# Kernel tuning notes

Measured on AMD Instinct MI355X. Metric: run time of the kernel, lower is better.

The kernel has to match this reference:

```python
import jax, jax.numpy as jnp
import numpy as np

DIM = 3072
NUM_HEADS = 24
HEAD_DIM = 128
INNER = NUM_HEADS * HEAD_DIM
EPS = 1e-5


def _layernorm(x, eps=EPS):
    # affine-free LayerNorm over the last (head_dim) axis
    mu = jnp.mean(x, axis=-1, keepdims=True)
    var = jnp.mean(jnp.square(x - mu), axis=-1, keepdims=True)
    return (x - mu) * jax.lax.rsqrt(var + eps)


def _rope_interleaved(x, cos, sin):
    # x: (B, S_img, H, D); cos/sin: (S_img, D//2). Non-neox (interleaved) style.
    x1 = x[..., 0::2]
    x2 = x[..., 1::2]
    c = cos[None, :, None, :]
    s = sin[None, :, None, :]
    o1 = x1 * c - x2 * s
    o2 = x2 * c + x1 * s
    return jnp.stack([o1, o2], axis=-1).reshape(x.shape)


def setup_inputs() -> dict:
    key = jax.random.key(0)
    ks = jax.random.split(key, 8)
    B, S_txt, S_img = 1, 256, 2048
    hidden_states = jax.random.normal(ks[0], (B, S_img, DIM), dtype=jnp.float32)
    encoder_hidden_states = jax.random.normal(ks[1], (B, S_txt, DIM), dtype=jnp.float32)
    cos = jax.random.uniform(ks[2], (S_img, HEAD_DIM // 2), dtype=jnp.float32)
    sin = jax.random.uniform(ks[3], (S_img, HEAD_DIM // 2), dtype=jnp.float32)
    Wqkv = jax.random.normal(ks[4], (DIM, 3 * INNER), dtype=jnp.float32) * (DIM ** -0.5)
    bqkv = jnp.zeros((3 * INNER,), dtype=jnp.float32)
    Wout = jax.random.normal(ks[5], (INNER, DIM), dtype=jnp.float32) * (INNER ** -0.5)
    bout = jnp.zeros((DIM,), dtype=jnp.float32)
    return {
        "hidden_states": hidden_states,
        "encoder_hidden_states": encoder_hidden_states,
        "cos": cos,
        "sin": sin,
        "Wqkv": Wqkv,
        "bqkv": bqkv,
        "Wout": Wout,
        "bout": bout,
        "text_seq_length": 256,
    }


def reference(hidden_states, encoder_hidden_states, cos, sin, Wqkv, bqkv, Wout, bout, text_seq_length):
    T = text_seq_length
    x = jnp.concatenate([encoder_hidden_states, hidden_states], axis=1)  # (B, S, dim)
    B, S, _ = x.shape
    qkv = x @ Wqkv + bqkv  # (B, S, 3*inner)
    q, k, v = jnp.split(qkv, 3, axis=-1)
    q = q.reshape(B, S, NUM_HEADS, HEAD_DIM)
    k = k.reshape(B, S, NUM_HEADS, HEAD_DIM)
    v = v.reshape(B, S, NUM_HEADS, HEAD_DIM)
    q = _layernorm(q)
    k = _layernorm(k)
    # partial RoPE: only on image-token slice
    q = jnp.concatenate([q[:, :T], _rope_interleaved(q[:, T:], cos, sin)], axis=1)
    k = jnp.concatenate([k[:, :T], _rope_interleaved(k[:, T:], cos, sin)], axis=1)
    scale = 1.0 / (HEAD_DIM ** 0.5)
    scores = jnp.einsum("bqhd,bkhd->bhqk", q, k) * scale
    probs = jax.nn.softmax(scores, axis=-1)
    out = jnp.einsum("bhqk,bkhd->bqhd", probs, v)
    out = out.reshape(B, S, INNER)
    out = out @ Wout + bout
    encoder_out = out[:, :T, :]
    hidden_out = out[:, T:, :]
    return (hidden_out, encoder_out)
```

## Files before the change

kernel.cpp:

```cpp
#include <hip/hip_runtime.h>

#define DIMC 3072
#define NH 24
#define HD 128
#define QKV_N 9216
#define S_TXT 256
#define S_IMG 2048
#define S_TOT 2304

typedef _Float16 f16x8 __attribute__((ext_vector_type(8)));
typedef _Float16 f16x4 __attribute__((ext_vector_type(4)));
typedef _Float16 f16x2 __attribute__((ext_vector_type(2)));
typedef float f32x4 __attribute__((ext_vector_type(4)));

#define MFMA(A, B, C) __builtin_amdgcn_mfma_f32_16x16x32_f16(A, B, C, 0, 0, 0)

#define QSCALE (0.08838834764831845f * 1.4426950408889634f)

__device__ __forceinline__ void gl2lds16(const _Float16* g, _Float16* l) {
    __builtin_amdgcn_global_load_lds(
        (const __attribute__((address_space(1))) unsigned int*)g,
        (__attribute__((address_space(3))) unsigned int*)l,
        16, 0, 0);
}

__global__ __launch_bounds__(256) void split_x(
    const float* __restrict__ enc, const float* __restrict__ hid,
    _Float16* __restrict__ xh)
{
    const int s = blockIdx.x;
    const float* src = (s < S_TXT) ? enc + (size_t)s * DIMC
                                   : hid + (size_t)(s - S_TXT) * DIMC;
    const int t = threadIdx.x;
#pragma unroll
    for (int it = 0; it < 3; ++it) {
        const int i = (it * 256 + t) * 4;
        float4 v = *(const float4*)(src + i);
        f16x4 hv;
        hv.x = (_Float16)v.x; hv.y = (_Float16)v.y;
        hv.z = (_Float16)v.z; hv.w = (_Float16)v.w;
        *(f16x4*)(xh + (size_t)s * DIMC + i) = hv;
    }
}

__global__ __launch_bounds__(256) void transpose_w_hi(
    const float* __restrict__ W, const int ldw, _Float16* __restrict__ Th)
{
    __shared__ float T[64][68];
    const int n0 = blockIdx.x * 64, k0 = blockIdx.y * 64;
    const int t = threadIdx.x;
    {
        const int r = t >> 2, c4 = (t & 3) * 16;
#pragma unroll
        for (int j = 0; j < 4; ++j) {
            float4 v = *(const float4*)(W + (size_t)(k0 + r) * ldw + n0 + c4 + j * 4);
            *(float4*)&T[r][c4 + j * 4] = v;
        }
    }
    __syncthreads();
    const int nr = t >> 2, kp = (t & 3) * 16;
    f16x8 hv0, hv1;
#pragma unroll
    for (int j = 0; j < 8; ++j) hv0[j] = (_Float16)T[kp + j][nr];
#pragma unroll
    for (int j = 0; j < 8; ++j) hv1[j] = (_Float16)T[kp + 8 + j][nr];
    _Float16* dh = Th + (size_t)(n0 + nr) * DIMC + k0 + kp;
    *(f16x8*)(dh) = hv0; *(f16x8*)(dh + 8) = hv1;
}

template <int REMAP>
__global__ __launch_bounds__(256) void gemm_f16_lds(
    const _Float16* __restrict__ Ah, const _Float16* __restrict__ Bh,
    const float* __restrict__ bias, float* __restrict__ C,
    const int nblk_m, const int ldc)
{
    __shared__ __attribute__((aligned(16))) _Float16 Ash[128 * 32];
    __shared__ __attribute__((aligned(16))) _Float16 Bsh[128 * 32];

    const int cpx = (int)gridDim.x >> 3;
    const int wgid = (blockIdx.x & 7) * cpx + (blockIdx.x >> 3);
    const int bm = (wgid % nblk_m) * 128;
    const int bn = (wgid / nblk_m) * 128;

    const int tid = threadIdx.x;
    const int l = tid & 63, w = tid >> 6;
    const int wr = w >> 1, wc = w & 1;
    const int lr = l & 15, g = l >> 4;

    const int srow0 = w * 32 + (l >> 2);
    const int srow1 = srow0 + 16;
    const int skp0 = (((l & 3) ^ ((srow0 >> 1) & 3)) * 8);
    const int skp1 = (((l & 3) ^ ((srow1 >> 1) & 3)) * 8);
    const _Float16* gA0 = Ah + (size_t)(bm + srow0) * DIMC + skp0;
    const _Float16* gA1 = Ah + (size_t)(bm + srow1) * DIMC + skp1;
    const _Float16* gB0 = Bh + (size_t)(bn + srow0) * DIMC + skp0;
    const _Float16* gB1 = Bh + (size_t)(bn + srow1) * DIMC + skp1;
    _Float16* lA0 = &Ash[(w * 32) * 32];
    _Float16* lA1 = &Ash[(w * 32 + 16) * 32];
    _Float16* lB0 = &Bsh[(w * 32) * 32];
    _Float16* lB1 = &Bsh[(w * 32 + 16) * 32];

    int aoff[4], boff[4];
#pragma unroll
    for (int i = 0; i < 4; ++i) {
        const int ra = wr * 64 + i * 16 + lr;
        const int rb = wc * 64 + i * 16 + lr;
        aoff[i] = ra * 32 + ((g ^ ((ra >> 1) & 3)) * 8);
        boff[i] = rb * 32 + ((g ^ ((rb >> 1) & 3)) * 8);
    }

    f32x4 acc[4][4] = {};

    for (int k0 = 0; k0 < DIMC; k0 += 32) {
        gl2lds16(gA0 + k0, lA0);
        gl2lds16(gA1 + k0, lA1);
        gl2lds16(gB0 + k0, lB0);
        gl2lds16(gB1 + k0, lB1);
        __syncthreads();

        f16x8 bhf[4];
#pragma unroll
        for (int ni = 0; ni < 4; ++ni)
            bhf[ni] = *(const f16x8*)&Bsh[boff[ni]];
#pragma unroll
        for (int mi = 0; mi < 4; ++mi) {
            f16x8 ahf = *(const f16x8*)&Ash[aoff[mi]];
#pragma unroll
            for (int ni = 0; ni < 4; ++ni)
                acc[mi][ni] = MFMA(ahf, bhf[ni], acc[mi][ni]);
        }
        __syncthreads();
    }

#pragma unroll
    for (int mi = 0; mi < 4; ++mi)
#pragma unroll
        for (int ni = 0; ni < 4; ++ni) {
            const int cl = bn + wc * 64 + ni * 16 + lr;
            const float bv = bias[cl];
#pragma unroll
            for (int e = 0; e < 4; ++e) {
                const int r = bm + wr * 64 + mi * 16 + g * 4 + e;
                if (REMAP) {
                    const int gr = (r < S_TXT) ? (S_IMG + r) : (r - S_TXT);
                    C[(size_t)gr * DIMC + cl] = acc[mi][ni][e] + bv;
                } else {
                    C[(size_t)r * ldc + cl] = acc[mi][ni][e] + bv;
                }
            }
        }
}

__global__ __launch_bounds__(256) void ln_rope_split(
    const float* __restrict__ qkv,
    const float* __restrict__ cost, const float* __restrict__ sint,
    _Float16* __restrict__ Qh, _Float16* __restrict__ Kh)
{
    const int wave = threadIdx.x >> 6;
    const int lane = threadIdx.x & 63;
    const int task = blockIdx.x * 4 + wave;
    const int s = task / 48;
    const int rem = task % 48;
    const int qk = rem / 24;
    const int h = rem % 24;

    const float* p = qkv + (size_t)s * QKV_N + qk * DIMC + h * HD;
    float2 x = *(const float2*)(p + lane * 2);

    float sum = x.x + x.y;
    float sq = x.x * x.x + x.y * x.y;
#pragma unroll
    for (int off = 1; off < 64; off <<= 1) {
        sum += __shfl_xor(sum, off, 64);
        sq  += __shfl_xor(sq, off, 64);
    }
    const float mu = sum * (1.0f / 128.0f);
    const float var = sq * (1.0f / 128.0f) - mu * mu;
    const float rstd = rsqrtf(var + 1e-5f);
    float y0 = (x.x - mu) * rstd;
    float y1 = (x.y - mu) * rstd;

    if (s >= S_TXT) {
        const int ip = s - S_TXT;
        const float c = cost[ip * 64 + lane];
        const float sn = sint[ip * 64 + lane];
        const float o0 = y0 * c - y1 * sn;
        const float o1 = y1 * c + y0 * sn;
        y0 = o0; y1 = o1;
    }
    if (qk == 0) { y0 *= QSCALE; y1 *= QSCALE; }

    const size_t off = ((size_t)h * S_TOT + s) * HD + lane * 2;
    f16x2 hv; hv.x = (_Float16)y0; hv.y = (_Float16)y1;
    *(f16x2*)((qk ? Kh : Qh) + off) = hv;
}

__global__ __launch_bounds__(256) void v_split_transpose(
    const float* __restrict__ qkv, _Float16* __restrict__ Vth)
{
    __shared__ float T[64][132];
    const int h = blockIdx.y;
    const int s0 = blockIdx.x * 64;
    const int t = threadIdx.x;
    {
        const int sl = t >> 2, dp = (t & 3) * 32;
#pragma unroll
        for (int j = 0; j < 8; ++j) {
            float4 v = *(const float4*)(qkv + (size_t)(s0 + sl) * QKV_N + 2 * DIMC + h * HD + dp + j * 4);
            *(float4*)&T[sl][dp + j * 4] = v;
        }
    }
    __syncthreads();
    const int d = t >> 1, sh = (t & 1) * 32;
    f16x8 hv[4];
#pragma unroll
    for (int ss = 0; ss < 32; ++ss)
        hv[ss >> 3][ss & 7] = (_Float16)T[sh + ss][d];
    _Float16* bh = Vth + ((size_t)h * HD + d) * S_TOT + s0 + sh;
#pragma unroll
    for (int j = 0; j < 4; ++j)
        *(f16x8*)(bh + j * 8) = hv[j];
}

__global__ __launch_bounds__(256) void attn_mfma(
    const _Float16* __restrict__ Qg, const _Float16* __restrict__ Kg,
    const _Float16* __restrict__ Vg, _Float16* __restrict__ aoh)
{
    __shared__ __attribute__((aligned(16))) _Float16 Ksh[4][64][40];
    __shared__ __attribute__((aligned(16))) _Float16 Vsh[128][80];
    __shared__ __attribute__((aligned(16))) _Float16 Pah[4][16][80];

    const int h = blockIdx.y;
    const int q0 = blockIdx.x * 64;
    const int tid = threadIdx.x;
    const int w = tid >> 6, l = tid & 63;
    const int lr = l & 15, g = l >> 4, lk = g * 8;

    const int qrow = q0 + w * 16 + lr;
    const _Float16* qb = Qg + ((size_t)h * S_TOT + qrow) * HD + lk;
    f16x8 qh[4];
#pragma unroll
    for (int db = 0; db < 4; ++db)
        qh[db] = *(const f16x8*)(qb + db * 32);

    f32x4 o[8] = {};
    float mrow = -3.0e38f, lrow = 0.0f;

    const int kkv = tid >> 2, kdb = tid & 3;
    const int vd = tid >> 1, vkh = (tid & 1) * 32;
    const _Float16* gK = Kg + ((size_t)h * S_TOT + kkv) * HD + kdb * 32;
    const _Float16* gV = Vg + ((size_t)h * HD + vd) * S_TOT + vkh;

    uint4 rK0, rK1, rK2, rK3, rV0, rV1, rV2, rV3;
#define LOADKV(kv0) { \
    rK0 = *(const uint4*)(gK + (size_t)(kv0) * HD);      rK1 = *(const uint4*)(gK + (size_t)(kv0) * HD + 8); \
    rK2 = *(const uint4*)(gK + (size_t)(kv0) * HD + 16); rK3 = *(const uint4*)(gK + (size_t)(kv0) * HD + 24); \
    rV0 = *(const uint4*)(gV + (kv0));      rV1 = *(const uint4*)(gV + (kv0) + 8); \
    rV2 = *(const uint4*)(gV + (kv0) + 16); rV3 = *(const uint4*)(gV + (kv0) + 24); }

    LOADKV(0);

    for (int kb = 0; kb < S_TOT / 64; ++kb) {
        __syncthreads();
        *(uint4*)&Ksh[kdb][kkv][0]  = rK0; *(uint4*)&Ksh[kdb][kkv][8]  = rK1;
        *(uint4*)&Ksh[kdb][kkv][16] = rK2; *(uint4*)&Ksh[kdb][kkv][24] = rK3;
        *(uint4*)&Vsh[vd][vkh]      = rV0; *(uint4*)&Vsh[vd][vkh + 8]  = rV1;
        *(uint4*)&Vsh[vd][vkh + 16] = rV2; *(uint4*)&Vsh[vd][vkh + 24] = rV3;
        __syncthreads();
        if (kb + 1 < S_TOT / 64) LOADKV((kb + 1) * 64);

        f32x4 sT[4] = {};
        __builtin_amdgcn_s_setprio(1);
#pragma unroll
        for (int db = 0; db < 4; ++db)
#pragma unroll
            for (int mf = 0; mf < 4; ++mf) {
                f16x8 kf = *(const f16x8*)&Ksh[db][mf * 16 + lr][lk];
                sT[mf] = MFMA(kf, qh[db], sT[mf]);
            }
        __builtin_amdgcn_s_setprio(0);

        float pm = -3.0e38f;
#pragma unroll
        for (int mf = 0; mf < 4; ++mf)
#pragma unroll
            for (int e = 0; e < 4; ++e)
                pm = fmaxf(pm, sT[mf][e]);
        pm = fmaxf(pm, __shfl_xor(pm, 16, 64));
        pm = fmaxf(pm, __shfl_xor(pm, 32, 64));

        if (__any(pm > mrow + 11.0f)) {
            const float mnew = fmaxf(mrow, pm);
            const float alpha = exp2f(mrow - mnew);
            lrow *= alpha;
            mrow = mnew;
            const float a0 = __shfl(alpha, g * 4 + 0, 64);
            const float a1 = __shfl(alpha, g * 4 + 1, 64);
            const float a2 = __shfl(alpha, g * 4 + 2, 64);
            const float a3 = __shfl(alpha, g * 4 + 3, 64);
#pragma unroll
            for (int df = 0; df < 8; ++df) {
                o[df][0] *= a0; o[df][1] *= a1; o[df][2] *= a2; o[df][3] *= a3;
            }
        }

        float rs = 0.0f;
        float ex_[4][4];
#pragma unroll
        for (int mf = 0; mf < 4; ++mf)
#pragma unroll
            for (int e = 0; e < 4; ++e) {
                const float pv = exp2f(sT[mf][e] - mrow);
                ex_[mf][e] = pv;
                rs += pv;
            }
        rs += __shfl_xor(rs, 16, 64);
        rs += __shfl_xor(rs, 32, 64);
        lrow += rs;

#pragma unroll
        for (int mf = 0; mf < 4; ++mf) {
            const int kvb = mf * 16 + g * 4;
            f16x2 t0; t0.x = (_Float16)ex_[mf][0]; t0.y = (_Float16)ex_[mf][1];
            f16x2 t1; t1.x = (_Float16)ex_[mf][2]; t1.y = (_Float16)ex_[mf][3];
            *(f16x2*)&Pah[w][lr][kvb] = t0;
            *(f16x2*)&Pah[w][lr][kvb + 2] = t1;
        }

        f16x8 pa0 = *(const f16x8*)&Pah[w][lr][lk];
        f16x8 pa1 = *(const f16x8*)&Pah[w][lr][32 + lk];
        __builtin_amdgcn_s_setprio(1);
#pragma unroll
        for (int df = 0; df < 8; ++df) {
            f16x8 vf0 = *(const f16x8*)&Vsh[df * 16 + lr][lk];
            f16x8 vf1 = *(const f16x8*)&Vsh[df * 16 + lr][32 + lk];
            o[df] = MFMA(pa0, vf0, o[df]);
            o[df] = MFMA(pa1, vf1, o[df]);
        }
        __builtin_amdgcn_s_setprio(0);
    }
#undef LOADKV

    const float inv = 1.0f / lrow;
    const float b0 = __shfl(inv, g * 4 + 0, 64);
    const float b1 = __shfl(inv, g * 4 + 1, 64);
    const float b2 = __shfl(inv, g * 4 + 2, 64);
    const float b3 = __shfl(inv, g * 4 + 3, 64);
    const float bb[4] = {b0, b1, b2, b3};
#pragma unroll
    for (int df = 0; df < 8; ++df)
#pragma unroll
        for (int e = 0; e < 4; ++e) {
            const int r = q0 + w * 16 + g * 4 + e;
            aoh[(size_t)r * DIMC + h * HD + df * 16 + lr] = (_Float16)(o[df][e] * bb[e]);
        }
}

extern "C" void kernel_launch(void* const* d_in, const int* in_sizes, int n_in,
                              void* d_out, int out_size, void* d_ws, size_t ws_size,
                              hipStream_t stream)
{
    const float* hid  = (const float*)d_in[0];
    const float* enc  = (const float*)d_in[1];
    const float* cost = (const float*)d_in[2];
    const float* sint = (const float*)d_in[3];
    const float* Wqkv = (const float*)d_in[4];
    const float* bqkv = (const float*)d_in[5];
    const float* Wout = (const float*)d_in[6];
    const float* bout = (const float*)d_in[7];
    float* out = (float*)d_out;

    char* ws = (char*)d_ws;
    float*    qkv  = (float*)(ws + 0);
    _Float16* aoh  = (_Float16*)(ws + 0);
    _Float16* xh   = (_Float16*)(ws + 84934656);
    _Float16* Qh   = (_Float16*)(ws + 84934656);
    _Float16* Kh   = (_Float16*)(ws + 99090432);
    _Float16* Wth  = (_Float16*)(ws + 113246208);
    _Float16* Vth  = (_Float16*)(ws + 113246208);
    _Float16* W2h  = (_Float16*)(ws + 132120576);

    split_x<<<S_TOT, 256, 0, stream>>>(enc, hid, xh);
    transpose_w_hi<<<dim3(144, 48), 256, 0, stream>>>(Wqkv, QKV_N, Wth);
    gemm_f16_lds<0><<<18 * 72, 256, 0, stream>>>(xh, Wth, bqkv, qkv, 18, QKV_N);
    transpose_w_hi<<<dim3(48, 48), 256, 0, stream>>>(Wout, DIMC, W2h);
    ln_rope_split<<<(S_TOT * 48) / 4, 256, 0, stream>>>(qkv, cost, sint, Qh, Kh);
    v_split_transpose<<<dim3(36, 24), 256, 0, stream>>>(qkv, Vth);
    attn_mfma<<<dim3(36, 24), 256, 0, stream>>>(Qh, Kh, Vth, aoh);
    gemm_f16_lds<1><<<18 * 24, 256, 0, stream>>>(aoh, W2h, bout, out, 18, DIMC);
}
```

Baseline: 477.4 us.

## Swizzle attention LDS layouts with XOR and remap blocks across XCDs

Replaces the padded K, V and P shared-memory arrays with unpadded arrays that use an XOR swizzle on 16-byte chunks. This avoids bank conflicts while cutting LDS footprint, which may allow more resident blocks per CU. It also flattens the grid to 1D and remaps block IDs so consecutive blocks of the same head land on the same XCD, to improve L2 reuse of K/V. The swizzle index math adds a few integer ops per access.

```diff
diff --git a/kernel.cpp b/kernel.cpp
--- a/kernel.cpp
+++ b/kernel.cpp
@@ -226,18 +226,19 @@
     const _Float16* __restrict__ Qg, const _Float16* __restrict__ Kg,
     const _Float16* __restrict__ Vg, _Float16* __restrict__ aoh)
 {
-    __shared__ __attribute__((aligned(16))) _Float16 Ksh[4][64][40];
-    __shared__ __attribute__((aligned(16))) _Float16 Vsh[128][80];
-    __shared__ __attribute__((aligned(16))) _Float16 Pah[4][16][80];
-
-    const int h = blockIdx.y;
-    const int q0 = blockIdx.x * 64;
+    __shared__ __attribute__((aligned(16))) _Float16 Ksh[4 * 64 * 32];
+    __shared__ __attribute__((aligned(16))) _Float16 Vsh[128 * 64];
+    __shared__ __attribute__((aligned(16))) _Float16 Pah[4 * 16 * 64];
+
+    const int wgid = ((int)blockIdx.x & 7) * 108 + ((int)blockIdx.x >> 3);
+    const int h = wgid / 36;
+    const int q0 = (wgid % 36) * 64;
     const int tid = threadIdx.x;
     const int w = tid >> 6, l = tid & 63;
-    const int lr = l & 15, g = l >> 4, lk = g * 8;
+    const int lr = l & 15, g = l >> 4;
 
     const int qrow = q0 + w * 16 + lr;
-    const _Float16* qb = Qg + ((size_t)h * S_TOT + qrow) * HD + lk;
+    const _Float16* qb = Qg + ((size_t)h * S_TOT + qrow) * HD + g * 8;
     f16x8 qh[4];
 #pragma unroll
     for (int db = 0; db < 4; ++db)
@@ -246,10 +247,23 @@
     f32x4 o[8] = {};
     float mrow = -3.0e38f, lrow = 0.0f;
 
+    const int kxr = (lr >> 1) & 3;
+    const int px  = lr & 7;
+    int ksl[4];
+#pragma unroll
+    for (int db = 0; db < 4; ++db) ksl[db] = (g ^ kxr ^ db) * 8;
+    const int vs0 = (g ^ px) * 8;
+    const int vs1 = ((4 + g) ^ px) * 8;
+
     const int kkv = tid >> 2, kdb = tid & 3;
-    const int vd = tid >> 1, vkh = (tid & 1) * 32;
+    const int vd = tid >> 1;
+    const int kx = (kkv >> 1) & 3;
+    const int kbase = kdb * 2048 + kkv * 32;
+    const int vbase = vd * 64;
+    const int vx = vd & 7;
+    const int vg0 = (tid & 1) * 4;
     const _Float16* gK = Kg + ((size_t)h * S_TOT + kkv) * HD + kdb * 32;
-    const _Float16* gV = Vg + ((size_t)h * HD + vd) * S_TOT + vkh;
+    const _Float16* gV = Vg + ((size_t)h * HD + vd) * S_TOT + (tid & 1) * 32;
 
     uint4 rK0, rK1, rK2, rK3, rV0, rV1, rV2, rV3;
 #define LOADKV(kv0) { \
@@ -262,10 +276,14 @@
 
     for (int kb = 0; kb < S_TOT / 64; ++kb) {
         __syncthreads();
-        *(uint4*)&Ksh[kdb][kkv][0]  = rK0; *(uint4*)&Ksh[kdb][kkv][8]  = rK1;
-        *(uint4*)&Ksh[kdb][kkv][16] = rK2; *(uint4*)&Ksh[kdb][kkv][24] = rK3;
-        *(uint4*)&Vsh[vd][vkh]      = rV0; *(uint4*)&Vsh[vd][vkh + 8]  = rV1;
-        *(uint4*)&Vsh[vd][vkh + 16] = rV2; *(uint4*)&Vsh[vd][vkh + 24] = rV3;
+        *(uint4*)&Ksh[kbase + ((0 ^ kx ^ kdb) * 8)] = rK0;
+        *(uint4*)&Ksh[kbase + ((1 ^ kx ^ kdb) * 8)] = rK1;
+        *(uint4*)&Ksh[kbase + ((2 ^ kx ^ kdb) * 8)] = rK2;
+        *(uint4*)&Ksh[kbase + ((3 ^ kx ^ kdb) * 8)] = rK3;
+        *(uint4*)&Vsh[vbase + (((vg0 + 0) ^ vx) * 8)] = rV0;
+        *(uint4*)&Vsh[vbase + (((vg0 + 1) ^ vx) * 8)] = rV1;
+        *(uint4*)&Vsh[vbase + (((vg0 + 2) ^ vx) * 8)] = rV2;
+        *(uint4*)&Vsh[vbase + (((vg0 + 3) ^ vx) * 8)] = rV3;
         __syncthreads();
         if (kb + 1 < S_TOT / 64) LOADKV((kb + 1) * 64);
 
@@ -275,7 +293,7 @@
         for (int db = 0; db < 4; ++db)
 #pragma unroll
             for (int mf = 0; mf < 4; ++mf) {
-                f16x8 kf = *(const f16x8*)&Ksh[db][mf * 16 + lr][lk];
+                f16x8 kf = *(const f16x8*)&Ksh[db * 2048 + (mf * 16 + lr) * 32 + ksl[db]];
                 sT[mf] = MFMA(kf, qh[db], sT[mf]);
             }
         __builtin_amdgcn_s_setprio(0);
@@ -318,22 +336,25 @@
         rs += __shfl_xor(rs, 32, 64);
         lrow += rs;
 
-#pragma unroll
-        for (int mf = 0; mf < 4; ++mf) {
-            const int kvb = mf * 16 + g * 4;
-            f16x2 t0; t0.x = (_Float16)ex_[mf][0]; t0.y = (_Float16)ex_[mf][1];
-            f16x2 t1; t1.x = (_Float16)ex_[mf][2]; t1.y = (_Float16)ex_[mf][3];
-            *(f16x2*)&Pah[w][lr][kvb] = t0;
-            *(f16x2*)&Pah[w][lr][kvb + 2] = t1;
-        }
-
-        f16x8 pa0 = *(const f16x8*)&Pah[w][lr][lk];
-        f16x8 pa1 = *(const f16x8*)&Pah[w][lr][32 + lk];
+        {
+            const int pbase = w * 1024 + lr * 64;
+#pragma unroll
+            for (int mf = 0; mf < 4; ++mf) {
+                const int slot = ((mf * 2 + (g >> 1)) ^ px) * 8 + (g & 1) * 4;
+                f16x2 t0; t0.x = (_Float16)ex_[mf][0]; t0.y = (_Float16)ex_[mf][1];
+                f16x2 t1; t1.x = (_Float16)ex_[mf][2]; t1.y = (_Float16)ex_[mf][3];
+                *(f16x2*)&Pah[pbase + slot]     = t0;
+                *(f16x2*)&Pah[pbase + slot + 2] = t1;
+            }
+        }
+
+        f16x8 pa0 = *(const f16x8*)&Pah[w * 1024 + lr * 64 + vs0];
+        f16x8 pa1 = *(const f16x8*)&Pah[w * 1024 + lr * 64 + vs1];
         __builtin_amdgcn_s_setprio(1);
 #pragma unroll
         for (int df = 0; df < 8; ++df) {
-            f16x8 vf0 = *(const f16x8*)&Vsh[df * 16 + lr][lk];
-            f16x8 vf1 = *(const f16x8*)&Vsh[df * 16 + lr][32 + lk];
+            f16x8 vf0 = *(const f16x8*)&Vsh[(df * 16 + lr) * 64 + vs0];
+            f16x8 vf1 = *(const f16x8*)&Vsh[(df * 16 + lr) * 64 + vs1];
             o[df] = MFMA(pa0, vf0, o[df]);
             o[df] = MFMA(pa1, vf1, o[df]);
         }
@@ -386,6 +407,6 @@
     transpose_w_hi<<<dim3(48, 48), 256, 0, stream>>>(Wout, DIMC, W2h);
     ln_rope_split<<<(S_TOT * 48) / 4, 256, 0, stream>>>(qkv, cost, sint, Qh, Kh);
     v_split_transpose<<<dim3(36, 24), 256, 0, stream>>>(qkv, Vth);
-    attn_mfma<<<dim3(36, 24), 256, 0, stream>>>(Qh, Kh, Vth, aoh);
+    attn_mfma<<<864, 256, 0, stream>>>(Qh, Kh, Vth, aoh);
     gemm_f16_lds<1><<<18 * 24, 256, 0, stream>>>(aoh, W2h, bout, out, 18, DIMC);
 }
```

Result: faster. 464.1 us (-2.8%).
